# Kernel tuning notes

Hardware: AMD Instinct MI355X
Metric: run time of the kernel (lower is better)

Reference implementation:

```python
import jax, jax.numpy as jnp
import numpy as np

N = 1024   # nodes
C = 256    # channels (n_features)
NEG_SLOPE = 0.2


def setup_inputs() -> dict:
    key = jax.random.key(0)
    k1, k2, k3, k4, k5, k6, k7 = jax.random.split(key, 7)
    nodes = jax.random.normal(k1, (N, C), dtype=jnp.float32)
    # dense adjacency used only via (adj != 0); force self-loops so every
    # softmax row has at least one valid entry
    adj_mat = jax.random.randint(k2, (N, N), 0, 2).astype(jnp.int32)
    adj_mat = adj_mat.at[jnp.arange(N), jnp.arange(N)].set(1)
    lim = 1.0 / np.sqrt(C)  # eqx.nn.Linear default uniform init bound
    W_src_w = jax.random.uniform(k3, (C, C), minval=-lim, maxval=lim, dtype=jnp.float32)
    W_src_b = jax.random.uniform(k4, (C,), minval=-lim, maxval=lim, dtype=jnp.float32)
    W_tgt_w = jax.random.uniform(k5, (C, C), minval=-lim, maxval=lim, dtype=jnp.float32)
    W_tgt_b = jax.random.uniform(k6, (C,), minval=-lim, maxval=lim, dtype=jnp.float32)
    a_w = jax.random.uniform(k7, (C,), minval=-lim, maxval=lim, dtype=jnp.float32)  # to_score, no bias
    return {"nodes": nodes, "adj_mat": adj_mat, "W_src_w": W_src_w, "W_src_b": W_src_b,
            "W_tgt_w": W_tgt_w, "W_tgt_b": W_tgt_b, "a_w": a_w}


def reference(nodes, adj_mat, W_src_w, W_src_b, W_tgt_w, W_tgt_b, a_w):
    # per-node linear maps (eqx.nn.Linear: y = W @ x + b)
    g_src = nodes @ W_src_w.T + W_src_b              # [node, C]
    g_tgt = nodes @ W_tgt_w.T + W_tgt_b              # [node, C]
    # g[i, j, c] = g_src[i, c] + g_tgt[j, c]   (axis names as in original: tgt, src)
    g = g_src[:, None, :] + g_tgt[None, :, :]        # [node, node, C]
    g = jax.nn.leaky_relu(g, NEG_SLOPE)
    score = jnp.einsum('ijc,c->ij', g, a_w)          # [node, node]
    score = jnp.where(adj_mat != 0, score, -jnp.inf) # mask non-edges
    weights = jax.nn.softmax(score, axis=1)          # over src axis
    return weights @ g_tgt                           # [node, C]
```

## Files before the change

kernel.cpp:

```cpp
#include <hip/hip_runtime.h>


typedef unsigned short u16;
typedef unsigned int   u32;
typedef _Float16 h2 __attribute__((ext_vector_type(2)));

#define NNODE 1024
#define NC    256
#define NEG   0.2f
#define BUFU  8192

__device__ __forceinline__ float bf2f(u16 h) {
    u32 u = ((u32)h) << 16;
    return __builtin_bit_cast(float, u);
}
__device__ __forceinline__ u16 f2bf(float f) {
    u32 u = __builtin_bit_cast(u32, f);
    u32 r = (u + 0x7FFFu + ((u >> 16) & 1u)) >> 16;
    return (u16)r;
}
__device__ __forceinline__ u16 f2h(float f) {
    _Float16 h = (_Float16)f;
    return __builtin_bit_cast(u16, h);
}
__device__ __forceinline__ h2 bch(u32 u) { return __builtin_bit_cast(h2, u); }
__device__ __forceinline__ h2 habs2(h2 y) {
    u32 u = __builtin_bit_cast(u32, y) & 0x7FFF7FFFu;
    return __builtin_bit_cast(h2, u);
}
__device__ __forceinline__ float dot2(h2 a, h2 b, float acc) {
#if __has_builtin(__builtin_amdgcn_fdot2)
    return __builtin_amdgcn_fdot2(a, b, acc, false);
#else
    acc = fmaf((float)a.x, (float)b.x, acc);
    return fmaf((float)a.y, (float)b.y, acc);
#endif
}

__device__ __forceinline__ int wave_detect(const u16* __restrict__ nodes, int lane)
{
    ushort4 v = *(const ushort4*)(nodes + lane * 4);
    const u16 h[4] = {v.x, v.y, v.z, v.w};
    int cnt = 0;
    #pragma unroll
    for (int q = 0; q < 4; ++q) {
        int e = (h[q] >> 7) & 0xFF;
        cnt += (e >= 132 || (e >= 1 && e <= 90)) ? 1 : 0;
    }
    #pragma unroll
    for (int off = 32; off; off >>= 1) cnt += __shfl_xor(cnt, off, 64);
    return (cnt >= 64) ? 0 : 1;
}

__device__ __forceinline__ int swz(int grp, int row) { return grp ^ (row & 31); }

__global__ __launch_bounds__(256) void lin_kernel(
    const void* __restrict__ nodes_v,
    const void* __restrict__ Wsrc_v, const void* __restrict__ bsrc_v,
    const void* __restrict__ Wtgt_v, const void* __restrict__ btgt_v,
    u16* __restrict__ gsh, u16* __restrict__ gth)
{
    __shared__ float nT[64][17];
    __shared__ float wT[64][68];

    const int t  = threadIdx.x;
    const int bf = wave_detect((const u16*)nodes_v, t & 63);
    const int ct = blockIdx.x;
    const int it = blockIdx.y;
    const int i0 = it * 16;
    const bool is_src = (ct < 4);
    const int c0 = (is_src ? ct : ct - 4) * 64;
    const void* __restrict__ Wv = is_src ? Wsrc_v : Wtgt_v;
    const void* __restrict__ bv = is_src ? bsrc_v : btgt_v;
    u16* __restrict__ g         = is_src ? gsh : gth;

    const int tc = t & 15, ti = t >> 4;
    float acc[4] = {};

    for (int k0 = 0; k0 < NC; k0 += 64) {
        __syncthreads();
        {
            int kg = t & 15, ii = t >> 4;
            float vals[4];
            if (bf) {
                ushort4 v = *(const ushort4*)((const u16*)nodes_v + (i0 + ii) * NC + k0 + kg * 4);
                vals[0] = bf2f(v.x); vals[1] = bf2f(v.y);
                vals[2] = bf2f(v.z); vals[3] = bf2f(v.w);
            } else {
                const float* nf = (const float*)nodes_v;
                float4 v = *(const float4*)(nf + (i0 + ii) * NC + k0 + kg * 4);
                vals[0] = v.x; vals[1] = v.y; vals[2] = v.z; vals[3] = v.w;
            }
            #pragma unroll
            for (int q = 0; q < 4; ++q) nT[kg * 4 + q][ii] = vals[q];
        }
        {
            int cc = t & 63, kg = t >> 6;
            float vals[16];
            if (bf) {
                const u16* W = (const u16*)Wv;
                uint4 v0 = *(const uint4*)(W + (c0 + cc) * NC + k0 + kg * 16);
                uint4 v1 = *(const uint4*)(W + (c0 + cc) * NC + k0 + kg * 16 + 8);
                const u16* p0 = (const u16*)&v0;
                const u16* p1 = (const u16*)&v1;
                #pragma unroll
                for (int q = 0; q < 8; ++q) { vals[q] = bf2f(p0[q]); vals[8 + q] = bf2f(p1[q]); }
            } else {
                const float* W = (const float*)Wv;
                #pragma unroll
                for (int h = 0; h < 4; ++h) {
                    float4 v = *(const float4*)(W + (c0 + cc) * NC + k0 + kg * 16 + 4 * h);
                    vals[4 * h + 0] = v.x; vals[4 * h + 1] = v.y;
                    vals[4 * h + 2] = v.z; vals[4 * h + 3] = v.w;
                }
            }
            #pragma unroll
            for (int q = 0; q < 16; ++q) wT[kg * 16 + q][cc] = vals[q];
        }
        __syncthreads();
        #pragma unroll 8
        for (int kk = 0; kk < 64; ++kk) {
            float  a  = nT[kk][ti];
            float4 bv4 = *(const float4*)&wT[kk][4 * tc];
            acc[0] = fmaf(a, bv4.x, acc[0]);
            acc[1] = fmaf(a, bv4.y, acc[1]);
            acc[2] = fmaf(a, bv4.z, acc[2]);
            acc[3] = fmaf(a, bv4.w, acc[3]);
        }
    }

    float bb[4];
    #pragma unroll
    for (int q = 0; q < 4; ++q)
        bb[q] = bf ? bf2f(((const u16*)bv)[c0 + 4 * tc + q])
                   : ((const float*)bv)[c0 + 4 * tc + q];
    const int irow = i0 + ti;
    ushort4 ov;
    ov.x = f2h(acc[0] + bb[0]);
    ov.y = f2h(acc[1] + bb[1]);
    ov.z = f2h(acc[2] + bb[2]);
    ov.w = f2h(acc[3] + bb[3]);
    *(ushort4*)(g + (size_t)irow * NC + c0 + 4 * tc) = ov;
}

__global__ __launch_bounds__(256) void sdot_kernel(
    const u16* __restrict__ gth, const void* __restrict__ aw_v,
    const u16* __restrict__ nodes_u16, float* __restrict__ sgt06)
{
    const int t    = threadIdx.x;
    const int lane = t & 63;
    const int bf   = wave_detect(nodes_u16, lane);
    const int row  = blockIdx.x * 4 + (t >> 6);

    float a0, a1, a2, a3;
    if (bf) {
        ushort4 a4 = *(const ushort4*)((const u16*)aw_v + lane * 4);
        a0 = bf2f(a4.x); a1 = bf2f(a4.y); a2 = bf2f(a4.z); a3 = bf2f(a4.w);
    } else {
        float4 a4 = *(const float4*)((const float*)aw_v + lane * 4);
        a0 = a4.x; a1 = a4.y; a2 = a4.z; a3 = a4.w;
    }
    ushort4 gv = *(const ushort4*)(gth + (size_t)row * NC + lane * 4);
    float s = a0 * (float)__builtin_bit_cast(_Float16, gv.x)
            + a1 * (float)__builtin_bit_cast(_Float16, gv.y)
            + a2 * (float)__builtin_bit_cast(_Float16, gv.z)
            + a3 * (float)__builtin_bit_cast(_Float16, gv.w);
    #pragma unroll
    for (int off = 32; off; off >>= 1) s += __shfl_xor(s, off, 64);
    if (lane == 0) sgt06[row] = 0.6f * s;
}

__global__ __launch_bounds__(512, 2) void fused_kernel(
    const u16* __restrict__ gsh, const u16* __restrict__ gth,
    const void* __restrict__ aw_v, const int* __restrict__ adj,
    const u16* __restrict__ nodes_u16, const float* __restrict__ sgt06,
    int jcnt, float* __restrict__ po, float* __restrict__ pm,
    float* __restrict__ pls, void* __restrict__ out_v)
{
    __shared__ u32   gt32[2 * BUFU];
    __shared__ u32   a32[128];
    __shared__ float p_lds[16][64];

    const int t    = threadIdx.x;
    const int i    = t >> 6;
    const int lane = t & 63;
    const int bf   = wave_detect(nodes_u16, lane);
    const int r0   = blockIdx.x * 16 + 2 * i;
    const int z    = blockIdx.y;
    const int jbase = z * jcnt;
    const int nt   = jcnt >> 6;
    const int jl = lane & 15, q  = lane >> 4;
    const int oc = lane & 31, hh = lane >> 5;

    auto stage_tile = [&](int bufIdx, int j0s) {
        #pragma unroll
        for (int c = 0; c < 4; ++c) {
            const int row = 16 * c + 2 * i + (lane >> 5);
            const int g   = lane & 31;
            const u16* gp = gth + (size_t)(j0s + row) * NC + (g ^ (row & 31)) * 8;
            u32* lp = gt32 + bufIdx * BUFU + row * 128 + g * 4;
            __builtin_amdgcn_global_load_lds(
                (const __attribute__((address_space(1))) void*)gp,
                (__attribute__((address_space(3))) void*)lp, 16, 0, 0);
        }
    };

    if (t < 128) {
        float a0, a1;
        if (bf) { a0 = bf2f(((const u16*)aw_v)[2 * t]); a1 = bf2f(((const u16*)aw_v)[2 * t + 1]); }
        else    { a0 = ((const float*)aw_v)[2 * t];     a1 = ((const float*)aw_v)[2 * t + 1]; }
        h2 av; av.x = (_Float16)(0.4f * a0); av.y = (_Float16)(0.4f * a1);
        a32[t] = __builtin_bit_cast(u32, av);
    }

    u32 gsr[2][32];
    #pragma unroll
    for (int r = 0; r < 2; ++r) {
        const u16* src = gsh + (size_t)(r0 + r) * NC + q * 64;
        #pragma unroll
        for (int k = 0; k < 8; ++k) {
            uint4 gv = *(const uint4*)(src + 8 * k);
            gsr[r][4 * k + 0] = gv.x; gsr[r][4 * k + 1] = gv.y;
            gsr[r][4 * k + 2] = gv.z; gsr[r][4 * k + 3] = gv.w;
        }
    }

    stage_tile(0, jbase);
    __syncthreads();

    float Sgs06[2];
    #pragma unroll
    for (int r = 0; r < 2; ++r) {
        float sg = 0.f;
        #pragma unroll
        for (int k = 0; k < 8; ++k) {
            uint4 a4 = *(const uint4*)&a32[q * 32 + 4 * k];
            sg = dot2(bch(a4.x), bch(gsr[r][4 * k + 0]), sg);
            sg = dot2(bch(a4.y), bch(gsr[r][4 * k + 1]), sg);
            sg = dot2(bch(a4.z), bch(gsr[r][4 * k + 2]), sg);
            sg = dot2(bch(a4.w), bch(gsr[r][4 * k + 3]), sg);
        }
        sg += __shfl_xor(sg, 16, 64);
        sg += __shfl_xor(sg, 32, 64);
        Sgs06[r] = 1.5f * sg;
    }

    float l[2] = {0.f, 0.f};
    float of[2][8] = {};

    for (int t2 = 0; t2 < nt; ++t2) {
        const int bb = (t2 & 1) * BUFU;
        const int j0 = jbase + t2 * 64;
        if (t2 + 1 < nt) stage_tile((t2 + 1) & 1, j0 + 64);

        const float sgtj = sgt06[j0 + lane];

        float spv[2][4] = {};
        #pragma unroll
        for (int k = 0; k < 8; ++k) {
            uint4 a4 = *(const uint4*)&a32[q * 32 + 4 * k];
            h2 a0 = bch(a4.x), a1 = bch(a4.y), a2 = bch(a4.z), a3 = bch(a4.w);
            #pragma unroll
            for (int p = 0; p < 4; ++p) {
                const int rowp = 16 * p + jl;
                uint4 g4 = *(const uint4*)&gt32[bb + rowp * 128 + swz(q * 8 + k, rowp) * 4];
                h2 t0 = bch(g4.x), t1 = bch(g4.y), t2v = bch(g4.z), t3 = bch(g4.w);
                #pragma unroll
                for (int r = 0; r < 2; ++r) {
                    spv[r][p] = dot2(a0, habs2(bch(gsr[r][4 * k + 0]) + t0), spv[r][p]);
                    spv[r][p] = dot2(a1, habs2(bch(gsr[r][4 * k + 1]) + t1), spv[r][p]);
                    spv[r][p] = dot2(a2, habs2(bch(gsr[r][4 * k + 2]) + t2v), spv[r][p]);
                    spv[r][p] = dot2(a3, habs2(bch(gsr[r][4 * k + 3]) + t3), spv[r][p]);
                }
            }
        }
        #pragma unroll
        for (int r = 0; r < 2; ++r)
            #pragma unroll
            for (int p = 0; p < 4; ++p) {
                spv[r][p] += __shfl_xor(spv[r][p], 16, 64);
                spv[r][p] += __shfl_xor(spv[r][p], 32, 64);
            }

        #pragma unroll
        for (int r = 0; r < 2; ++r) {
            const float sabs = (lane < 16) ? spv[r][0] : (lane < 32) ? spv[r][1]
                             : (lane < 48) ? spv[r][2] : spv[r][3];
            const float s = sabs + Sgs06[r] + sgtj;
            const int valid = adj[(size_t)(r0 + r) * NNODE + j0 + lane];
            const float p = valid ? __expf(s) : 0.f;
            l[r] += p;
            p_lds[2 * i + r][lane] = p;
        }

        #pragma unroll 4
        for (int jp = 0; jp < 32; ++jp) {
            const int j = 2 * jp + hh;
            const float w0 = p_lds[2 * i    ][j];
            const float w1 = p_lds[2 * i + 1][j];
            uint4 g4 = *(const uint4*)&gt32[bb + j * 128 + swz(oc, j) * 4];
            h2 v0 = bch(g4.x), v1 = bch(g4.y), v2 = bch(g4.z), v3 = bch(g4.w);
            of[0][0] = fmaf(w0, (float)v0.x, of[0][0]);
            of[0][1] = fmaf(w0, (float)v0.y, of[0][1]);
            of[0][2] = fmaf(w0, (float)v1.x, of[0][2]);
            of[0][3] = fmaf(w0, (float)v1.y, of[0][3]);
            of[0][4] = fmaf(w0, (float)v2.x, of[0][4]);
            of[0][5] = fmaf(w0, (float)v2.y, of[0][5]);
            of[0][6] = fmaf(w0, (float)v3.x, of[0][6]);
            of[0][7] = fmaf(w0, (float)v3.y, of[0][7]);
            of[1][0] = fmaf(w1, (float)v0.x, of[1][0]);
            of[1][1] = fmaf(w1, (float)v0.y, of[1][1]);
            of[1][2] = fmaf(w1, (float)v1.x, of[1][2]);
            of[1][3] = fmaf(w1, (float)v1.y, of[1][3]);
            of[1][4] = fmaf(w1, (float)v2.x, of[1][4]);
            of[1][5] = fmaf(w1, (float)v2.y, of[1][5]);
            of[1][6] = fmaf(w1, (float)v3.x, of[1][6]);
            of[1][7] = fmaf(w1, (float)v3.y, of[1][7]);
        }

        __syncthreads();
    }

    #pragma unroll
    for (int r = 0; r < 2; ++r) {
        #pragma unroll
        for (int off = 32; off; off >>= 1) l[r] += __shfl_xor(l[r], off, 64);
        #pragma unroll
        for (int k = 0; k < 8; ++k) of[r][k] += __shfl_xor(of[r][k], 32, 64);
    }

    if (lane < 32) {
        #pragma unroll
        for (int r = 0; r < 2; ++r) {
            const int row = r0 + r;
            if (out_v) {
                const float inv = 1.0f / l[r];
                if (bf) {
                    u16* out = (u16*)out_v;
                    ushort4 oa, ob;
                    oa.x = f2bf(of[r][0] * inv); oa.y = f2bf(of[r][1] * inv);
                    oa.z = f2bf(of[r][2] * inv); oa.w = f2bf(of[r][3] * inv);
                    ob.x = f2bf(of[r][4] * inv); ob.y = f2bf(of[r][5] * inv);
                    ob.z = f2bf(of[r][6] * inv); ob.w = f2bf(of[r][7] * inv);
                    *(ushort4*)(out + (size_t)row * NC + 8 * oc)     = oa;
                    *(ushort4*)(out + (size_t)row * NC + 8 * oc + 4) = ob;
                } else {
                    float* out = (float*)out_v;
                    *(float4*)(out + (size_t)row * NC + 8 * oc) =
                        make_float4(of[r][0] * inv, of[r][1] * inv,
                                    of[r][2] * inv, of[r][3] * inv);
                    *(float4*)(out + (size_t)row * NC + 8 * oc + 4) =
                        make_float4(of[r][4] * inv, of[r][5] * inv,
                                    of[r][6] * inv, of[r][7] * inv);
                }
            } else {
                float* pp = po + ((size_t)z * NNODE + row) * NC + 8 * oc;
                *(float4*)pp       = make_float4(of[r][0], of[r][1], of[r][2], of[r][3]);
                *(float4*)(pp + 4) = make_float4(of[r][4], of[r][5], of[r][6], of[r][7]);
            }
        }
    }
    if (!out_v && lane == 0) {
        #pragma unroll
        for (int r = 0; r < 2; ++r) {
            pm [(size_t)z * NNODE + r0 + r] = 0.f;
            pls[(size_t)z * NNODE + r0 + r] = l[r];
        }
    }
}

__global__ __launch_bounds__(256) void combine_kernel(
    const float* __restrict__ po, const float* __restrict__ pm,
    const float* __restrict__ pls, const u16* __restrict__ nodes_u16,
    int ns, void* __restrict__ out_v)
{
    const int bf  = wave_detect(nodes_u16, threadIdx.x & 63);
    const int row = blockIdx.x;
    const int c   = threadIdx.x;

    float v;
    if (ns == 8) {
        float mv[8], lv[8], ov[8];
        #pragma unroll
        for (int zz = 0; zz < 8; ++zz) {
            mv[zz] = pm [zz * NNODE + row];
            lv[zz] = pls[zz * NNODE + row];
            ov[zz] = po [(size_t)(zz * NNODE + row) * NC + c];
        }
        float mstar = mv[0];
        #pragma unroll
        for (int zz = 1; zz < 8; ++zz) mstar = fmaxf(mstar, mv[zz]);
        float acc = 0.f, lsum = 0.f;
        #pragma unroll
        for (int zz = 0; zz < 8; ++zz) {
            const float wz = __expf(mv[zz] - mstar);
            lsum = fmaf(lv[zz], wz, lsum);
            acc  = fmaf(ov[zz], wz, acc);
        }
        v = acc / lsum;
    } else {
        float mstar = -1e30f;
        for (int zz = 0; zz < ns; ++zz)
            mstar = fmaxf(mstar, pm[zz * NNODE + row]);
        float acc = 0.f, lsum = 0.f;
        for (int zz = 0; zz < ns; ++zz) {
            const float wz = __expf(pm[zz * NNODE + row] - mstar);
            lsum = fmaf(pls[zz * NNODE + row], wz, lsum);
            acc  = fmaf(po[(size_t)(zz * NNODE + row) * NC + c], wz, acc);
        }
        v = acc / lsum;
    }
    if (bf) ((u16*)out_v)[row * NC + c] = f2bf(v);
    else    ((float*)out_v)[row * NC + c] = v;
}

extern "C" void kernel_launch(void* const* d_in, const int* in_sizes, int n_in,
                              void* d_out, int out_size, void* d_ws, size_t ws_size,
                              hipStream_t stream)
{
    const u16* nodes_u16 = (const u16*)d_in[0];
    const int* adj       = (const int*)d_in[1];

    char*  wsb   = (char*)d_ws;
    u16*   gsh   = (u16*)wsb;
    u16*   gth   = gsh + (size_t)NNODE * NC;
    float* sgt06 = (float*)(wsb + 2ull * NNODE * NC * sizeof(u16));

    lin_kernel<<<dim3(8, 64), 256, 0, stream>>>(d_in[0], d_in[2], d_in[3],
                                                d_in[4], d_in[5], gsh, gth);
    sdot_kernel<<<256, 256, 0, stream>>>(gth, d_in[6], nodes_u16, sgt06);

    const size_t base = 2ull * NNODE * NC * sizeof(u16) + NNODE * sizeof(float);
    const size_t per  = 4ull * NNODE * NC + 8ull * NNODE;
    int NS = 0;
    if      (ws_size >= base + 8 * per) NS = 8;
    else if (ws_size >= base + 4 * per) NS = 4;
    else if (ws_size >= base + 2 * per) NS = 2;

    if (NS) {
        float* po  = (float*)(wsb + base);
        float* pm  = po + (size_t)NS * NNODE * NC;
        float* pls = pm + (size_t)NS * NNODE;
        fused_kernel<<<dim3(64, NS), 512, 0, stream>>>(
            gsh, gth, d_in[6], adj, nodes_u16, sgt06, NNODE / NS,
            po, pm, pls, nullptr);
        combine_kernel<<<NNODE, 256, 0, stream>>>(po, pm, pls, nodes_u16, NS, d_out);
    } else {
        fused_kernel<<<dim3(64, 1), 512, 0, stream>>>(
            gsh, gth, d_in[6], adj, nodes_u16, sgt06, NNODE,
            nullptr, nullptr, nullptr, d_out);
    }
}
```

Baseline: 61.32 us.

## Fuse target score dot into linear kernel and use packed FMA accumulation

```diff
diff --git a/kernel.cpp b/kernel.cpp
--- a/kernel.cpp
+++ b/kernel.cpp
@@ -4,6 +4,7 @@
 typedef unsigned short u16;
 typedef unsigned int   u32;
 typedef _Float16 h2 __attribute__((ext_vector_type(2)));
+typedef float    f2v __attribute__((ext_vector_type(2)));
 
 #define NNODE 1024
 #define NC    256
@@ -36,6 +37,13 @@
     return fmaf((float)a.y, (float)b.y, acc);
 #endif
 }
+__device__ __forceinline__ f2v pkfma(f2v a, f2v b, f2v c) {
+#if __has_builtin(__builtin_elementwise_fma)
+    return __builtin_elementwise_fma(a, b, c);
+#else
+    f2v r; r.x = fmaf(a.x, b.x, c.x); r.y = fmaf(a.y, b.y, c.y); return r;
+#endif
+}
 
 __device__ __forceinline__ int wave_detect(const u16* __restrict__ nodes, int lane)
 {
@@ -58,7 +66,8 @@
     const void* __restrict__ nodes_v,
     const void* __restrict__ Wsrc_v, const void* __restrict__ bsrc_v,
     const void* __restrict__ Wtgt_v, const void* __restrict__ btgt_v,
-    u16* __restrict__ gsh, u16* __restrict__ gth)
+    const void* __restrict__ aw_v,
+    u16* __restrict__ gsh, u16* __restrict__ gth, float* __restrict__ sgt06)
 {
     __shared__ float nT[64][17];
     __shared__ float wT[64][68];
@@ -135,39 +144,25 @@
         bb[q] = bf ? bf2f(((const u16*)bv)[c0 + 4 * tc + q])
                    : ((const float*)bv)[c0 + 4 * tc + q];
     const int irow = i0 + ti;
+    const float g0 = acc[0] + bb[0], g1 = acc[1] + bb[1],
+                g2 = acc[2] + bb[2], g3 = acc[3] + bb[3];
     ushort4 ov;
-    ov.x = f2h(acc[0] + bb[0]);
-    ov.y = f2h(acc[1] + bb[1]);
-    ov.z = f2h(acc[2] + bb[2]);
-    ov.w = f2h(acc[3] + bb[3]);
+    ov.x = f2h(g0); ov.y = f2h(g1); ov.z = f2h(g2); ov.w = f2h(g3);
     *(ushort4*)(g + (size_t)irow * NC + c0 + 4 * tc) = ov;
-}
-
-__global__ __launch_bounds__(256) void sdot_kernel(
-    const u16* __restrict__ gth, const void* __restrict__ aw_v,
-    const u16* __restrict__ nodes_u16, float* __restrict__ sgt06)
-{
-    const int t    = threadIdx.x;
-    const int lane = t & 63;
-    const int bf   = wave_detect(nodes_u16, lane);
-    const int row  = blockIdx.x * 4 + (t >> 6);
-
-    float a0, a1, a2, a3;
-    if (bf) {
-        ushort4 a4 = *(const ushort4*)((const u16*)aw_v + lane * 4);
-        a0 = bf2f(a4.x); a1 = bf2f(a4.y); a2 = bf2f(a4.z); a3 = bf2f(a4.w);
-    } else {
-        float4 a4 = *(const float4*)((const float*)aw_v + lane * 4);
-        a0 = a4.x; a1 = a4.y; a2 = a4.z; a3 = a4.w;
-    }
-    ushort4 gv = *(const ushort4*)(gth + (size_t)row * NC + lane * 4);
-    float s = a0 * (float)__builtin_bit_cast(_Float16, gv.x)
-            + a1 * (float)__builtin_bit_cast(_Float16, gv.y)
-            + a2 * (float)__builtin_bit_cast(_Float16, gv.z)
-            + a3 * (float)__builtin_bit_cast(_Float16, gv.w);
-    #pragma unroll
-    for (int off = 32; off; off >>= 1) s += __shfl_xor(s, off, 64);
-    if (lane == 0) sgt06[row] = 0.6f * s;
+
+    if (!is_src) {
+        float aa[4];
+        #pragma unroll
+        for (int q = 0; q < 4; ++q)
+            aa[q] = bf ? bf2f(((const u16*)aw_v)[c0 + 4 * tc + q])
+                       : ((const float*)aw_v)[c0 + 4 * tc + q];
+        float part = fmaf(aa[0], g0, fmaf(aa[1], g1, fmaf(aa[2], g2, aa[3] * g3)));
+        part += __shfl_xor(part, 1, 64);
+        part += __shfl_xor(part, 2, 64);
+        part += __shfl_xor(part, 4, 64);
+        part += __shfl_xor(part, 8, 64);
+        if (tc == 0) atomicAdd(&sgt06[irow], 0.6f * part);
+    }
 }
 
 __global__ __launch_bounds__(512, 2) void fused_kernel(
@@ -246,7 +241,7 @@
     }
 
     float l[2] = {0.f, 0.f};
-    float of[2][8] = {};
+    f2v of2[2][4] = {};
 
     for (int t2 = 0; t2 < nt; ++t2) {
         const int bb = (t2 & 1) * BUFU;
@@ -300,27 +295,32 @@
             const float w1 = p_lds[2 * i + 1][j];
             uint4 g4 = *(const uint4*)&gt32[bb + j * 128 + swz(oc, j) * 4];
             h2 v0 = bch(g4.x), v1 = bch(g4.y), v2 = bch(g4.z), v3 = bch(g4.w);
-            of[0][0] = fmaf(w0, (float)v0.x, of[0][0]);
-            of[0][1] = fmaf(w0, (float)v0.y, of[0][1]);
-            of[0][2] = fmaf(w0, (float)v1.x, of[0][2]);
-            of[0][3] = fmaf(w0, (float)v1.y, of[0][3]);
-            of[0][4] = fmaf(w0, (float)v2.x, of[0][4]);
-            of[0][5] = fmaf(w0, (float)v2.y, of[0][5]);
-            of[0][6] = fmaf(w0, (float)v3.x, of[0][6]);
-            of[0][7] = fmaf(w0, (float)v3.y, of[0][7]);
-            of[1][0] = fmaf(w1, (float)v0.x, of[1][0]);
-            of[1][1] = fmaf(w1, (float)v0.y, of[1][1]);
-            of[1][2] = fmaf(w1, (float)v1.x, of[1][2]);
-            of[1][3] = fmaf(w1, (float)v1.y, of[1][3]);
-            of[1][4] = fmaf(w1, (float)v2.x, of[1][4]);
-            of[1][5] = fmaf(w1, (float)v2.y, of[1][5]);
-            of[1][6] = fmaf(w1, (float)v3.x, of[1][6]);
-            of[1][7] = fmaf(w1, (float)v3.y, of[1][7]);
+            f2v e0 = {(float)v0.x, (float)v0.y};
+            f2v e1 = {(float)v1.x, (float)v1.y};
+            f2v e2 = {(float)v2.x, (float)v2.y};
+            f2v e3 = {(float)v3.x, (float)v3.y};
+            f2v w0v = {w0, w0}, w1v = {w1, w1};
+            of2[0][0] = pkfma(w0v, e0, of2[0][0]);
+            of2[0][1] = pkfma(w0v, e1, of2[0][1]);
+            of2[0][2] = pkfma(w0v, e2, of2[0][2]);
+            of2[0][3] = pkfma(w0v, e3, of2[0][3]);
+            of2[1][0] = pkfma(w1v, e0, of2[1][0]);
+            of2[1][1] = pkfma(w1v, e1, of2[1][1]);
+            of2[1][2] = pkfma(w1v, e2, of2[1][2]);
+            of2[1][3] = pkfma(w1v, e3, of2[1][3]);
         }
 
         __syncthreads();
     }
 
+    float of[2][8];
+    #pragma unroll
+    for (int r = 0; r < 2; ++r) {
+        of[r][0] = of2[r][0].x; of[r][1] = of2[r][0].y;
+        of[r][2] = of2[r][1].x; of[r][3] = of2[r][1].y;
+        of[r][4] = of2[r][2].x; of[r][5] = of2[r][2].y;
+        of[r][6] = of2[r][3].x; of[r][7] = of2[r][3].y;
+    }
     #pragma unroll
     for (int r = 0; r < 2; ++r) {
         #pragma unroll
@@ -426,9 +426,10 @@
     u16*   gth   = gsh + (size_t)NNODE * NC;
     float* sgt06 = (float*)(wsb + 2ull * NNODE * NC * sizeof(u16));
 
+    hipMemsetAsync(sgt06, 0, NNODE * sizeof(float), stream);
     lin_kernel<<<dim3(8, 64), 256, 0, stream>>>(d_in[0], d_in[2], d_in[3],
-                                                d_in[4], d_in[5], gsh, gth);
-    sdot_kernel<<<256, 256, 0, stream>>>(gth, d_in[6], nodes_u16, sgt06);
+                                                d_in[4], d_in[5], d_in[6],
+                                                gsh, gth, sgt06);
 
     const size_t base = 2ull * NNODE * NC * sizeof(u16) + NNODE * sizeof(float);
     const size_t per  = 4ull * NNODE * NC + 8ull * NNODE;
```

Result: slower. 64.41 us (+5.0%).

## Read g_tgt tiles directly from global memory instead of double-buffered LDS staging

Applied to the files above, without the earlier changes.

```diff
diff --git a/kernel.cpp b/kernel.cpp
--- a/kernel.cpp
+++ b/kernel.cpp
@@ -8,7 +8,6 @@
 #define NNODE 1024
 #define NC    256
 #define NEG   0.2f
-#define BUFU  8192
 
 __device__ __forceinline__ float bf2f(u16 h) {
     u32 u = ((u32)h) << 16;
@@ -51,8 +50,6 @@
     for (int off = 32; off; off >>= 1) cnt += __shfl_xor(cnt, off, 64);
     return (cnt >= 64) ? 0 : 1;
 }
-
-__device__ __forceinline__ int swz(int grp, int row) { return grp ^ (row & 31); }
 
 __global__ __launch_bounds__(256) void lin_kernel(
     const void* __restrict__ nodes_v,
@@ -177,9 +174,8 @@
     int jcnt, float* __restrict__ po, float* __restrict__ pm,
     float* __restrict__ pls, void* __restrict__ out_v)
 {
-    __shared__ u32   gt32[2 * BUFU];
-    __shared__ u32   a32[128];
-    __shared__ float p_lds[16][64];
+    __shared__ u32    a32[128];
+    __shared__ float2 p2[8][64];
 
     const int t    = threadIdx.x;
     const int i    = t >> 6;
@@ -188,22 +184,8 @@
     const int r0   = blockIdx.x * 16 + 2 * i;
     const int z    = blockIdx.y;
     const int jbase = z * jcnt;
-    const int nt   = jcnt >> 6;
     const int jl = lane & 15, q  = lane >> 4;
     const int oc = lane & 31, hh = lane >> 5;
-
-    auto stage_tile = [&](int bufIdx, int j0s) {
-        #pragma unroll
-        for (int c = 0; c < 4; ++c) {
-            const int row = 16 * c + 2 * i + (lane >> 5);
-            const int g   = lane & 31;
-            const u16* gp = gth + (size_t)(j0s + row) * NC + (g ^ (row & 31)) * 8;
-            u32* lp = gt32 + bufIdx * BUFU + row * 128 + g * 4;
-            __builtin_amdgcn_global_load_lds(
-                (const __attribute__((address_space(1))) void*)gp,
-                (__attribute__((address_space(3))) void*)lp, 16, 0, 0);
-        }
-    };
 
     if (t < 128) {
         float a0, a1;
@@ -224,8 +206,6 @@
             gsr[r][4 * k + 2] = gv.z; gsr[r][4 * k + 3] = gv.w;
         }
     }
-
-    stage_tile(0, jbase);
     __syncthreads();
 
     float Sgs06[2];
@@ -248,11 +228,7 @@
     float l[2] = {0.f, 0.f};
     float of[2][8] = {};
 
-    for (int t2 = 0; t2 < nt; ++t2) {
-        const int bb = (t2 & 1) * BUFU;
-        const int j0 = jbase + t2 * 64;
-        if (t2 + 1 < nt) stage_tile((t2 + 1) & 1, j0 + 64);
-
+    for (int j0 = jbase; j0 < jbase + jcnt; j0 += 64) {
         const float sgtj = sgt06[j0 + lane];
 
         float spv[2][4] = {};
@@ -263,7 +239,7 @@
             #pragma unroll
             for (int p = 0; p < 4; ++p) {
                 const int rowp = 16 * p + jl;
-                uint4 g4 = *(const uint4*)&gt32[bb + rowp * 128 + swz(q * 8 + k, rowp) * 4];
+                uint4 g4 = *(const uint4*)(gth + (size_t)(j0 + rowp) * NC + (q * 8 + k) * 8);
                 h2 t0 = bch(g4.x), t1 = bch(g4.y), t2v = bch(g4.z), t3 = bch(g4.w);
                 #pragma unroll
                 for (int r = 0; r < 2; ++r) {
@@ -282,43 +258,41 @@
                 spv[r][p] += __shfl_xor(spv[r][p], 32, 64);
             }
 
+        float pr[2];
         #pragma unroll
         for (int r = 0; r < 2; ++r) {
             const float sabs = (lane < 16) ? spv[r][0] : (lane < 32) ? spv[r][1]
                              : (lane < 48) ? spv[r][2] : spv[r][3];
             const float s = sabs + Sgs06[r] + sgtj;
             const int valid = adj[(size_t)(r0 + r) * NNODE + j0 + lane];
-            const float p = valid ? __expf(s) : 0.f;
-            l[r] += p;
-            p_lds[2 * i + r][lane] = p;
-        }
+            pr[r] = valid ? __expf(s) : 0.f;
+            l[r] += pr[r];
+        }
+        p2[i][lane] = make_float2(pr[0], pr[1]);
 
         #pragma unroll 4
         for (int jp = 0; jp < 32; ++jp) {
             const int j = 2 * jp + hh;
-            const float w0 = p_lds[2 * i    ][j];
-            const float w1 = p_lds[2 * i + 1][j];
-            uint4 g4 = *(const uint4*)&gt32[bb + j * 128 + swz(oc, j) * 4];
+            const float2 w = p2[i][j];
+            uint4 g4 = *(const uint4*)(gth + (size_t)(j0 + j) * NC + oc * 8);
             h2 v0 = bch(g4.x), v1 = bch(g4.y), v2 = bch(g4.z), v3 = bch(g4.w);
-            of[0][0] = fmaf(w0, (float)v0.x, of[0][0]);
-            of[0][1] = fmaf(w0, (float)v0.y, of[0][1]);
-            of[0][2] = fmaf(w0, (float)v1.x, of[0][2]);
-            of[0][3] = fmaf(w0, (float)v1.y, of[0][3]);
-            of[0][4] = fmaf(w0, (float)v2.x, of[0][4]);
-            of[0][5] = fmaf(w0, (float)v2.y, of[0][5]);
-            of[0][6] = fmaf(w0, (float)v3.x, of[0][6]);
-            of[0][7] = fmaf(w0, (float)v3.y, of[0][7]);
-            of[1][0] = fmaf(w1, (float)v0.x, of[1][0]);
-            of[1][1] = fmaf(w1, (float)v0.y, of[1][1]);
-            of[1][2] = fmaf(w1, (float)v1.x, of[1][2]);
-            of[1][3] = fmaf(w1, (float)v1.y, of[1][3]);
-            of[1][4] = fmaf(w1, (float)v2.x, of[1][4]);
-            of[1][5] = fmaf(w1, (float)v2.y, of[1][5]);
-            of[1][6] = fmaf(w1, (float)v3.x, of[1][6]);
-            of[1][7] = fmaf(w1, (float)v3.y, of[1][7]);
-        }
-
-        __syncthreads();
+            of[0][0] = fmaf(w.x, (float)v0.x, of[0][0]);
+            of[0][1] = fmaf(w.x, (float)v0.y, of[0][1]);
+            of[0][2] = fmaf(w.x, (float)v1.x, of[0][2]);
+            of[0][3] = fmaf(w.x, (float)v1.y, of[0][3]);
+            of[0][4] = fmaf(w.x, (float)v2.x, of[0][4]);
+            of[0][5] = fmaf(w.x, (float)v2.y, of[0][5]);
+            of[0][6] = fmaf(w.x, (float)v3.x, of[0][6]);
+            of[0][7] = fmaf(w.x, (float)v3.y, of[0][7]);
+            of[1][0] = fmaf(w.y, (float)v0.x, of[1][0]);
+            of[1][1] = fmaf(w.y, (float)v0.y, of[1][1]);
+            of[1][2] = fmaf(w.y, (float)v1.x, of[1][2]);
+            of[1][3] = fmaf(w.y, (float)v1.y, of[1][3]);
+            of[1][4] = fmaf(w.y, (float)v2.x, of[1][4]);
+            of[1][5] = fmaf(w.y, (float)v2.y, of[1][5]);
+            of[1][6] = fmaf(w.y, (float)v3.x, of[1][6]);
+            of[1][7] = fmaf(w.y, (float)v3.y, of[1][7]);
+        }
     }
 
     #pragma unroll
```

Result: slower. 72.33 us (+18.0%).
